# Kernel optimization log

Measured on AMD Instinct MI355X. Metric: run time of the kernel, lower is better.

## Reference

```python
import jax, jax.numpy as jnp
import numpy as np

N_USER = 100000
N_ITEM = 200000
N_NODES = N_USER + N_ITEM
NNZ = 4000000
EMB = 64
N_LAYERS = 3
BATCH = 4096


def setup_inputs() -> dict:
    key = jax.random.key(0)
    ks = jax.random.split(key, 12)
    inp = {
        'users': jax.random.randint(ks[0], (BATCH,), 0, N_USER, dtype=jnp.int32),
        'pos_items': jax.random.randint(ks[1], (BATCH,), 0, N_ITEM, dtype=jnp.int32),
        'neg_items': jax.random.randint(ks[2], (BATCH,), 0, N_ITEM, dtype=jnp.int32),
        'row': jax.random.randint(ks[3], (NNZ,), 0, N_NODES, dtype=jnp.int32),
        'col': jax.random.randint(ks[4], (NNZ,), 0, N_NODES, dtype=jnp.int32),
        'vals': jax.random.uniform(ks[5], (NNZ,), dtype=jnp.float32),
        'user_emb': 0.1 * jax.random.normal(ks[6], (N_USER, EMB), dtype=jnp.float32),
        'item_emb': 0.1 * jax.random.normal(ks[7], (N_ITEM, EMB), dtype=jnp.float32),
        'W_gc': 0.1 * jax.random.normal(ks[8], (N_LAYERS, EMB, EMB), dtype=jnp.float32),
        'b_gc': 0.1 * jax.random.normal(ks[9], (N_LAYERS, EMB), dtype=jnp.float32),
        'W_bi': 0.1 * jax.random.normal(ks[10], (N_LAYERS, EMB, EMB), dtype=jnp.float32),
        'b_bi': 0.1 * jax.random.normal(ks[11], (N_LAYERS, EMB), dtype=jnp.float32),
    }
    return inp


def _l2_normalize(x, eps=1e-12):
    # matches torch F.normalize(p=2, dim=1): x / max(||x||, eps)
    n = jnp.sqrt(jnp.sum(x * x, axis=1, keepdims=True))
    return x / jnp.maximum(n, eps)


def reference(users, pos_items, neg_items, row, col, vals, user_emb, item_emb, W_gc, b_gc, W_bi, b_bi):
    B = users.shape[0]
    # sparse adjacency propagation: side = A_hat @ [user_emb; item_emb]
    emb = jnp.concatenate([user_emb, item_emb], axis=0)          # [N, d]
    msgs = vals[:, None] * emb[col]                               # [nnz, d]
    side = jax.ops.segment_sum(msgs, row, num_segments=N_NODES)  # [N, d]

    u_side = side[users]                                          # [B, d]
    i_side = jnp.concatenate([side[N_USER + pos_items], side[N_USER + neg_items]], axis=0)
    small_side = jnp.concatenate([u_side, i_side], axis=0)        # [3B, d]
    ego = jnp.concatenate([user_emb[users], item_emb[pos_items], item_emb[neg_items]], axis=0)

    all_embeddings = [ego]
    for k in range(N_LAYERS):
        sum_e = small_side @ W_gc[k] + b_gc[k]
        bi = (ego * small_side) @ W_bi[k] + b_bi[k]
        ego = jax.nn.leaky_relu(sum_e + bi, negative_slope=0.2)
        all_embeddings.append(_l2_normalize(ego))

    all_e = jnp.concatenate(all_embeddings, axis=1)               # [3B, d*(L+1)]
    u_g = all_e[:B]
    i_g = all_e[B:]
    pos_g = i_g[:B]
    neg_g = i_g[B:]
    return (u_g, pos_g, neg_g)
```

## Files before the change

kernel.cpp:

```cpp
#include <hip/hip_runtime.h>

#define N_USER   100000
#define N_ITEM   200000
#define N_NODES  300000
#define NNZ      4000000
#define EMB      64
#define N_LAYERS 3
#define BATCH    4096
#define NSLOT    (3*BATCH)
#define MAXE     96


__global__ void k_setup(const int* __restrict__ users,
                        const int* __restrict__ pos,
                        const int* __restrict__ neg,
                        int* __restrict__ slot_of_node,
                        int* __restrict__ count) {
    int i = blockIdx.x * blockDim.x + threadIdx.x;
    if (i >= NSLOT) return;
    count[i] = 0;
    int node;
    if (i < BATCH)            node = users[i];
    else if (i < 2 * BATCH)   node = N_USER + pos[i - BATCH];
    else                      node = N_USER + neg[i - 2 * BATCH];
    slot_of_node[node] = i;
}

__global__ void __launch_bounds__(256) k_build(
        const int* __restrict__ row,
        const int* __restrict__ col,
        const float* __restrict__ vals,
        const int* __restrict__ slot_of_node,
        int* __restrict__ count,
        int* __restrict__ csr_col,
        float* __restrict__ csr_val) {
    int t = blockIdx.x * blockDim.x + threadIdx.x;
    if (t >= NNZ / 4) return;
    int4 r = ((const int4*)row)[t];
    int s0 = slot_of_node[r.x];
    int s1 = slot_of_node[r.y];
    int s2 = slot_of_node[r.z];
    int s3 = slot_of_node[r.w];
    int e = t * 4;
    if (s0 >= 0) { int p = atomicAdd(&count[s0], 1); if (p < MAXE) { csr_col[(size_t)s0*MAXE+p] = col[e];   csr_val[(size_t)s0*MAXE+p] = vals[e];   } }
    if (s1 >= 0) { int p = atomicAdd(&count[s1], 1); if (p < MAXE) { csr_col[(size_t)s1*MAXE+p] = col[e+1]; csr_val[(size_t)s1*MAXE+p] = vals[e+1]; } }
    if (s2 >= 0) { int p = atomicAdd(&count[s2], 1); if (p < MAXE) { csr_col[(size_t)s2*MAXE+p] = col[e+2]; csr_val[(size_t)s2*MAXE+p] = vals[e+2]; } }
    if (s3 >= 0) { int p = atomicAdd(&count[s3], 1); if (p < MAXE) { csr_col[(size_t)s3*MAXE+p] = col[e+3]; csr_val[(size_t)s3*MAXE+p] = vals[e+3]; } }
}

__global__ void __launch_bounds__(256) k_gather(
        const int* __restrict__ users,
        const int* __restrict__ pos,
        const int* __restrict__ neg,
        const float* __restrict__ user_emb,
        const float* __restrict__ item_emb,
        const int* __restrict__ slot_of_node,
        const int* __restrict__ count,
        const int* __restrict__ csr_col,
        const float* __restrict__ csr_val,
        float* __restrict__ side) {
    int tid = threadIdx.x;
    int w = tid >> 6;
    int j = tid & 63;
    int slot = blockIdx.x * 4 + w;

    int node;
    if (slot < BATCH)          node = users[slot];
    else if (slot < 2 * BATCH) node = N_USER + pos[slot - BATCH];
    else                       node = N_USER + neg[slot - 2 * BATCH];

    int wslot = slot_of_node[node];
    wslot = __builtin_amdgcn_readfirstlane(wslot);
    int n = count[wslot];
    n = (n < MAXE) ? n : MAXE;
    n = __builtin_amdgcn_readfirstlane(n);
    const int*   cc = csr_col + (size_t)wslot * MAXE;
    const float* cv = csr_val + (size_t)wslot * MAXE;

    float acc = 0.f;
    for (int t0 = 0; t0 < n; t0 += 8) {
        float vv[8];
        const float* ss[8];
        #pragma unroll
        for (int k = 0; k < 8; ++k) {
            int  t  = t0 + k;
            bool ok = t < n;
            int  idx = ok ? t : 0;
            int   c = cc[idx];
            float v = cv[idx];
            vv[k] = ok ? v : 0.f;
            ss[k] = (c < N_USER) ? (user_emb + (size_t)c * EMB)
                                 : (item_emb + (size_t)(c - N_USER) * EMB);
        }
        float gg[8];
        #pragma unroll
        for (int k = 0; k < 8; ++k) gg[k] = ss[k][j];
        #pragma unroll
        for (int k = 0; k < 8; ++k) acc = fmaf(vv[k], gg[k], acc);
    }
    side[(size_t)slot * EMB + j] = acc;
}

__global__ void __launch_bounds__(256) k_mlp(
        const int* __restrict__ users,
        const int* __restrict__ pos,
        const int* __restrict__ neg,
        const float* __restrict__ user_emb,
        const float* __restrict__ item_emb,
        const float* __restrict__ W_gc,
        const float* __restrict__ b_gc,
        const float* __restrict__ W_bi,
        const float* __restrict__ b_bi,
        const float* __restrict__ side,
        float* __restrict__ out) {
    __shared__ float wg[EMB * EMB];
    __shared__ float wb[EMB * EMB];
    int tid = threadIdx.x;
    int w = tid >> 6;
    int j = tid & 63;
    int sbase = blockIdx.x * 16 + w * 4;

    float sval[4], e[4];
    #pragma unroll
    for (int s = 0; s < 4; ++s) {
        int slot = sbase + s;
        int node;
        if (slot < BATCH)          node = users[slot];
        else if (slot < 2 * BATCH) node = N_USER + pos[slot - BATCH];
        else                       node = N_USER + neg[slot - 2 * BATCH];
        const float* erow = (node < N_USER) ? (user_emb + (size_t)node * EMB)
                                            : (item_emb + (size_t)(node - N_USER) * EMB);
        e[s]    = erow[j];
        sval[s] = side[(size_t)slot * EMB + j];
        out[(size_t)slot * 256 + j] = e[s];
    }

    for (int k = 0; k < N_LAYERS; ++k) {
        __syncthreads();
        {
            const float4* g4 = (const float4*)(W_gc + (size_t)k * EMB * EMB);
            const float4* b4 = (const float4*)(W_bi + (size_t)k * EMB * EMB);
            float4* lg = (float4*)wg;
            float4* lb = (float4*)wb;
            #pragma unroll
            for (int i2 = tid; i2 < EMB * EMB / 4; i2 += 256) { lg[i2] = g4[i2]; lb[i2] = b4[i2]; }
        }
        __syncthreads();

        float b1 = b_gc[k * EMB + j];
        float b2 = b_bi[k * EMB + j];
        float sum1[4], sum2[4], pv[4];
        #pragma unroll
        for (int s = 0; s < 4; ++s) { sum1[s] = b1; sum2[s] = b2; pv[s] = sval[s] * e[s]; }

        #pragma unroll 8
        for (int i = 0; i < EMB; ++i) {
            float wgi = wg[i * EMB + j];
            float wbi = wb[i * EMB + j];
            #pragma unroll
            for (int s = 0; s < 4; ++s) {
                float si = __uint_as_float(__builtin_amdgcn_readlane(__float_as_uint(sval[s]), i));
                float pi = __uint_as_float(__builtin_amdgcn_readlane(__float_as_uint(pv[s]),   i));
                sum1[s] = fmaf(si, wgi, sum1[s]);
                sum2[s] = fmaf(pi, wbi, sum2[s]);
            }
        }

        #pragma unroll
        for (int s = 0; s < 4; ++s) {
            float x = sum1[s] + sum2[s];
            x = (x >= 0.f) ? x : 0.2f * x;
            float sq = x * x;
            #pragma unroll
            for (int o = 32; o; o >>= 1) sq += __shfl_xor(sq, o, 64);
            float nn = fmaxf(sqrtf(sq), 1e-12f);
            out[(size_t)(sbase + s) * 256 + (k + 1) * 64 + j] = x / nn;
            e[s] = x;
        }
    }
}

extern "C" void kernel_launch(void* const* d_in, const int* in_sizes, int n_in,
                              void* d_out, int out_size, void* d_ws, size_t ws_size,
                              hipStream_t stream) {
    const int*   users    = (const int*)  d_in[0];
    const int*   pos      = (const int*)  d_in[1];
    const int*   neg      = (const int*)  d_in[2];
    const int*   row      = (const int*)  d_in[3];
    const int*   col      = (const int*)  d_in[4];
    const float* vals     = (const float*)d_in[5];
    const float* user_emb = (const float*)d_in[6];
    const float* item_emb = (const float*)d_in[7];
    const float* W_gc     = (const float*)d_in[8];
    const float* b_gc     = (const float*)d_in[9];
    const float* W_bi     = (const float*)d_in[10];
    const float* b_bi     = (const float*)d_in[11];
    float* out = (float*)d_out;

    char* ws = (char*)d_ws;
    int*   slot_of_node = (int*)ws;
    int*   count        = (int*)(ws + 1200128);
    int*   csr_col      = (int*)(ws + 1249280);
    float* csr_val      = (float*)(ws + 5967872);
    float* side         = (float*)(ws + 10686464);

    hipMemsetAsync(slot_of_node, 0xFF, (size_t)N_NODES * sizeof(int), stream);

    k_setup<<<(NSLOT + 255) / 256, 256, 0, stream>>>(users, pos, neg,
                                                     slot_of_node, count);
    k_build<<<(NNZ / 4 + 255) / 256, 256, 0, stream>>>(row, col, vals, slot_of_node,
                                                       count, csr_col, csr_val);
    k_gather<<<NSLOT / 4, 256, 0, stream>>>(users, pos, neg, user_emb, item_emb,
                                            slot_of_node, count, csr_col, csr_val,
                                            side);
    k_mlp<<<NSLOT / 16, 256, 0, stream>>>(users, pos, neg, user_emb, item_emb,
                                          W_gc, b_gc, W_bi, b_bi, side, out);
}
```

Measured before the change: 90.25 us.

## Filter edges with a shared-memory node bitmap and deepen gather unroll

```diff
diff --git a/kernel.cpp b/kernel.cpp
--- a/kernel.cpp
+++ b/kernel.cpp
@@ -9,13 +9,15 @@
 #define BATCH    4096
 #define NSLOT    (3*BATCH)
 #define MAXE     96
+#define BMWORDS  9376
 
 
 __global__ void k_setup(const int* __restrict__ users,
                         const int* __restrict__ pos,
                         const int* __restrict__ neg,
                         int* __restrict__ slot_of_node,
-                        int* __restrict__ count) {
+                        int* __restrict__ count,
+                        unsigned int* __restrict__ bitmap) {
     int i = blockIdx.x * blockDim.x + threadIdx.x;
     if (i >= NSLOT) return;
     count[i] = 0;
@@ -24,6 +26,7 @@
     else if (i < 2 * BATCH)   node = N_USER + pos[i - BATCH];
     else                      node = N_USER + neg[i - 2 * BATCH];
     slot_of_node[node] = i;
+    atomicOr(&bitmap[((unsigned)node) >> 5], 1u << (node & 31));
 }
 
 __global__ void __launch_bounds__(256) k_build(
@@ -31,21 +34,37 @@
         const int* __restrict__ col,
         const float* __restrict__ vals,
         const int* __restrict__ slot_of_node,
+        const unsigned int* __restrict__ bitmap,
         int* __restrict__ count,
         int* __restrict__ csr_col,
         float* __restrict__ csr_val) {
-    int t = blockIdx.x * blockDim.x + threadIdx.x;
-    if (t >= NNZ / 4) return;
-    int4 r = ((const int4*)row)[t];
-    int s0 = slot_of_node[r.x];
-    int s1 = slot_of_node[r.y];
-    int s2 = slot_of_node[r.z];
-    int s3 = slot_of_node[r.w];
-    int e = t * 4;
-    if (s0 >= 0) { int p = atomicAdd(&count[s0], 1); if (p < MAXE) { csr_col[(size_t)s0*MAXE+p] = col[e];   csr_val[(size_t)s0*MAXE+p] = vals[e];   } }
-    if (s1 >= 0) { int p = atomicAdd(&count[s1], 1); if (p < MAXE) { csr_col[(size_t)s1*MAXE+p] = col[e+1]; csr_val[(size_t)s1*MAXE+p] = vals[e+1]; } }
-    if (s2 >= 0) { int p = atomicAdd(&count[s2], 1); if (p < MAXE) { csr_col[(size_t)s2*MAXE+p] = col[e+2]; csr_val[(size_t)s2*MAXE+p] = vals[e+2]; } }
-    if (s3 >= 0) { int p = atomicAdd(&count[s3], 1); if (p < MAXE) { csr_col[(size_t)s3*MAXE+p] = col[e+3]; csr_val[(size_t)s3*MAXE+p] = vals[e+3]; } }
+    __shared__ unsigned int bm[BMWORDS];
+    int tid = threadIdx.x;
+    {
+        const int4* src = (const int4*)bitmap;
+        int4* dst = (int4*)bm;
+        for (int i = tid; i < BMWORDS / 4; i += 256) dst[i] = src[i];
+    }
+    __syncthreads();
+
+    const int4* rows4 = (const int4*)row;
+    int gbase = blockIdx.x * 512;
+    #pragma unroll
+    for (int q = 0; q < 2; ++q) {
+        int t = gbase + q * 256 + tid;
+        if (t < NNZ / 4) {
+            int4 r = rows4[t];
+            int e = t * 4;
+            bool h0 = (bm[((unsigned)r.x) >> 5] >> (r.x & 31)) & 1;
+            bool h1 = (bm[((unsigned)r.y) >> 5] >> (r.y & 31)) & 1;
+            bool h2 = (bm[((unsigned)r.z) >> 5] >> (r.z & 31)) & 1;
+            bool h3 = (bm[((unsigned)r.w) >> 5] >> (r.w & 31)) & 1;
+            if (h0) { int s = slot_of_node[r.x]; int p = atomicAdd(&count[s], 1); if (p < MAXE) { csr_col[(size_t)s*MAXE+p] = col[e];   csr_val[(size_t)s*MAXE+p] = vals[e];   } }
+            if (h1) { int s = slot_of_node[r.y]; int p = atomicAdd(&count[s], 1); if (p < MAXE) { csr_col[(size_t)s*MAXE+p] = col[e+1]; csr_val[(size_t)s*MAXE+p] = vals[e+1]; } }
+            if (h2) { int s = slot_of_node[r.z]; int p = atomicAdd(&count[s], 1); if (p < MAXE) { csr_col[(size_t)s*MAXE+p] = col[e+2]; csr_val[(size_t)s*MAXE+p] = vals[e+2]; } }
+            if (h3) { int s = slot_of_node[r.w]; int p = atomicAdd(&count[s], 1); if (p < MAXE) { csr_col[(size_t)s*MAXE+p] = col[e+3]; csr_val[(size_t)s*MAXE+p] = vals[e+3]; } }
+        }
+    }
 }
 
 __global__ void __launch_bounds__(256) k_gather(
@@ -78,11 +97,11 @@
     const float* cv = csr_val + (size_t)wslot * MAXE;
 
     float acc = 0.f;
-    for (int t0 = 0; t0 < n; t0 += 8) {
-        float vv[8];
-        const float* ss[8];
-        #pragma unroll
-        for (int k = 0; k < 8; ++k) {
+    for (int t0 = 0; t0 < n; t0 += 16) {
+        float vv[16];
+        const float* ss[16];
+        #pragma unroll
+        for (int k = 0; k < 16; ++k) {
             int  t  = t0 + k;
             bool ok = t < n;
             int  idx = ok ? t : 0;
@@ -92,11 +111,11 @@
             ss[k] = (c < N_USER) ? (user_emb + (size_t)c * EMB)
                                  : (item_emb + (size_t)(c - N_USER) * EMB);
         }
-        float gg[8];
-        #pragma unroll
-        for (int k = 0; k < 8; ++k) gg[k] = ss[k][j];
-        #pragma unroll
-        for (int k = 0; k < 8; ++k) acc = fmaf(vv[k], gg[k], acc);
+        float gg[16];
+        #pragma unroll
+        for (int k = 0; k < 16; ++k) gg[k] = ss[k][j];
+        #pragma unroll
+        for (int k = 0; k < 16; ++k) acc = fmaf(vv[k], gg[k], acc);
     }
     side[(size_t)slot * EMB + j] = acc;
 }
@@ -198,18 +217,20 @@
     float* out = (float*)d_out;
 
     char* ws = (char*)d_ws;
-    int*   slot_of_node = (int*)ws;
-    int*   count        = (int*)(ws + 1200128);
-    int*   csr_col      = (int*)(ws + 1249280);
-    float* csr_val      = (float*)(ws + 5967872);
-    float* side         = (float*)(ws + 10686464);
+    int*          slot_of_node = (int*)ws;
+    int*          count        = (int*)(ws + 1200128);
+    int*          csr_col      = (int*)(ws + 1249280);
+    float*        csr_val      = (float*)(ws + 5967872);
+    float*        side         = (float*)(ws + 10686464);
+    unsigned int* bitmap       = (unsigned int*)(ws + 13832192);
 
     hipMemsetAsync(slot_of_node, 0xFF, (size_t)N_NODES * sizeof(int), stream);
+    hipMemsetAsync(bitmap, 0, (size_t)BMWORDS * sizeof(unsigned int), stream);
 
     k_setup<<<(NSLOT + 255) / 256, 256, 0, stream>>>(users, pos, neg,
-                                                     slot_of_node, count);
-    k_build<<<(NNZ / 4 + 255) / 256, 256, 0, stream>>>(row, col, vals, slot_of_node,
-                                                       count, csr_col, csr_val);
+                                                     slot_of_node, count, bitmap);
+    k_build<<<(NNZ / 4 + 511) / 512, 256, 0, stream>>>(row, col, vals, slot_of_node,
+                                                       bitmap, count, csr_col, csr_val);
     k_gather<<<NSLOT / 4, 256, 0, stream>>>(users, pos, neg, user_emb, item_emb,
                                             slot_of_node, count, csr_col, csr_val,
                                             side);
```

Result: no change. 91.79 us (+1.7%).

## Compact matching edges in shared memory before scattering, widen gather unroll

Applied to the files above, without the earlier changes.

```diff
diff --git a/kernel.cpp b/kernel.cpp
--- a/kernel.cpp
+++ b/kernel.cpp
@@ -9,6 +9,7 @@
 #define BATCH    4096
 #define NSLOT    (3*BATCH)
 #define MAXE     96
+#define HCAP     768
 
 
 __global__ void k_setup(const int* __restrict__ users,
@@ -34,18 +35,66 @@
         int* __restrict__ count,
         int* __restrict__ csr_col,
         float* __restrict__ csr_val) {
-    int t = blockIdx.x * blockDim.x + threadIdx.x;
-    if (t >= NNZ / 4) return;
-    int4 r = ((const int4*)row)[t];
-    int s0 = slot_of_node[r.x];
-    int s1 = slot_of_node[r.y];
-    int s2 = slot_of_node[r.z];
-    int s3 = slot_of_node[r.w];
-    int e = t * 4;
-    if (s0 >= 0) { int p = atomicAdd(&count[s0], 1); if (p < MAXE) { csr_col[(size_t)s0*MAXE+p] = col[e];   csr_val[(size_t)s0*MAXE+p] = vals[e];   } }
-    if (s1 >= 0) { int p = atomicAdd(&count[s1], 1); if (p < MAXE) { csr_col[(size_t)s1*MAXE+p] = col[e+1]; csr_val[(size_t)s1*MAXE+p] = vals[e+1]; } }
-    if (s2 >= 0) { int p = atomicAdd(&count[s2], 1); if (p < MAXE) { csr_col[(size_t)s2*MAXE+p] = col[e+2]; csr_val[(size_t)s2*MAXE+p] = vals[e+2]; } }
-    if (s3 >= 0) { int p = atomicAdd(&count[s3], 1); if (p < MAXE) { csr_col[(size_t)s3*MAXE+p] = col[e+3]; csr_val[(size_t)s3*MAXE+p] = vals[e+3]; } }
+    __shared__ int ls_e[HCAP];
+    __shared__ int ls_s[HCAP];
+    __shared__ int cnt;
+    int tid = threadIdx.x;
+    if (tid == 0) cnt = 0;
+    __syncthreads();
+
+    const int4* rows4 = (const int4*)row;
+    const int nt4 = NNZ / 4;
+    int base4 = blockIdx.x * 1024;
+
+    int4 r[4]; bool ok[4];
+    #pragma unroll
+    for (int q = 0; q < 4; ++q) {
+        int t = base4 + q * 256 + tid;
+        ok[q] = t < nt4;
+        r[q] = rows4[ok[q] ? t : 0];
+    }
+    int s[16];
+    #pragma unroll
+    for (int q = 0; q < 4; ++q) {
+        s[q * 4 + 0] = slot_of_node[r[q].x];
+        s[q * 4 + 1] = slot_of_node[r[q].y];
+        s[q * 4 + 2] = slot_of_node[r[q].z];
+        s[q * 4 + 3] = slot_of_node[r[q].w];
+    }
+    #pragma unroll
+    for (int q = 0; q < 4; ++q) {
+        if (!ok[q]) continue;
+        int e = (base4 + q * 256 + tid) * 4;
+        #pragma unroll
+        for (int i = 0; i < 4; ++i) {
+            int si = s[q * 4 + i];
+            if (si >= 0) {
+                int p = atomicAdd(&cnt, 1);
+                if (p < HCAP) { ls_e[p] = e + i; ls_s[p] = si; }
+                else {
+                    int pp = atomicAdd(&count[si], 1);
+                    if (pp < MAXE) {
+                        csr_col[(size_t)si * MAXE + pp] = col[e + i];
+                        csr_val[(size_t)si * MAXE + pp] = vals[e + i];
+                    }
+                }
+            }
+        }
+    }
+    __syncthreads();
+
+    int n = cnt; n = (n < HCAP) ? n : HCAP;
+    for (int t = tid; t < n; t += 256) {
+        int e  = ls_e[t];
+        int si = ls_s[t];
+        int c  = col[e];
+        float v = vals[e];
+        int p = atomicAdd(&count[si], 1);
+        if (p < MAXE) {
+            csr_col[(size_t)si * MAXE + p] = c;
+            csr_val[(size_t)si * MAXE + p] = v;
+        }
+    }
 }
 
 __global__ void __launch_bounds__(256) k_gather(
@@ -78,25 +127,25 @@
     const float* cv = csr_val + (size_t)wslot * MAXE;
 
     float acc = 0.f;
-    for (int t0 = 0; t0 < n; t0 += 8) {
-        float vv[8];
-        const float* ss[8];
-        #pragma unroll
-        for (int k = 0; k < 8; ++k) {
+    for (int t0 = 0; t0 < n; t0 += 16) {
+        float vv[16];
+        const float* ss[16];
+        #pragma unroll
+        for (int k = 0; k < 16; ++k) {
             int  t  = t0 + k;
-            bool ok = t < n;
-            int  idx = ok ? t : 0;
+            bool okk = t < n;
+            int  idx = okk ? t : 0;
             int   c = cc[idx];
             float v = cv[idx];
-            vv[k] = ok ? v : 0.f;
+            vv[k] = okk ? v : 0.f;
             ss[k] = (c < N_USER) ? (user_emb + (size_t)c * EMB)
                                  : (item_emb + (size_t)(c - N_USER) * EMB);
         }
-        float gg[8];
-        #pragma unroll
-        for (int k = 0; k < 8; ++k) gg[k] = ss[k][j];
-        #pragma unroll
-        for (int k = 0; k < 8; ++k) acc = fmaf(vv[k], gg[k], acc);
+        float gg[16];
+        #pragma unroll
+        for (int k = 0; k < 16; ++k) gg[k] = ss[k][j];
+        #pragma unroll
+        for (int k = 0; k < 16; ++k) acc = fmaf(vv[k], gg[k], acc);
     }
     side[(size_t)slot * EMB + j] = acc;
 }
@@ -208,8 +257,8 @@
 
     k_setup<<<(NSLOT + 255) / 256, 256, 0, stream>>>(users, pos, neg,
                                                      slot_of_node, count);
-    k_build<<<(NNZ / 4 + 255) / 256, 256, 0, stream>>>(row, col, vals, slot_of_node,
-                                                       count, csr_col, csr_val);
+    k_build<<<(NNZ / 4 + 1023) / 1024, 256, 0, stream>>>(row, col, vals, slot_of_node,
+                                                         count, csr_col, csr_val);
     k_gather<<<NSLOT / 4, 256, 0, stream>>>(users, pos, neg, user_emb, item_emb,
                                             slot_of_node, count, csr_col, csr_val,
                                             side);
```

After: 88.83 us. Within noise of the previous version (-1.6%).
